# Kernel optimization log

Hardware: AMD Instinct MI355X
Metric: run time of the kernel (lower is better)

Reference implementation:

```python
import jax, jax.numpy as jnp
import numpy as np

K = 3          # kernel size
DIL = 1        # dilation
PAD = (K + (K - 1) * (DIL - 1)) // 2   # = 1
CENTER = (K * K - 1) // 2              # = 4
D_MIN = 0.0
D_MAX = 10.0
MIN_NGHBR = 4


def _unfold(x):
    """x: (B,C,H,W) -> patches (B,H,W,k*k,C), matching torch.nn.Unfold ordering."""
    b, c, h, w = x.shape
    xp = jnp.pad(x, ((0, 0), (0, 0), (PAD, PAD), (PAD, PAD)))
    # fixed k*k=9 taps: loop over the kernel window only (not data dims)
    pats = [xp[:, :, i * DIL:i * DIL + h, j * DIL:j * DIL + w]
            for i in range(K) for j in range(K)]
    p = jnp.stack(pats, axis=2)          # (B,C,kk,H,W)
    return p.transpose(0, 3, 4, 2, 1)    # (B,H,W,kk,C)


def setup_inputs() -> dict:
    key = jax.random.key(0)
    kxy, kz = jax.random.split(key)
    B, H, W = 4, 480, 640
    xy = jax.random.normal(kxy, (B, 2, H, W), dtype=jnp.float32)
    z = jax.random.uniform(kz, (B, 1, H, W), dtype=jnp.float32, minval=0.1, maxval=9.9)
    points = jnp.concatenate([xy, z], axis=1)  # (B,3,H,W)
    return {"points": points}


def reference(points):
    b, _, h, w = points.shape
    # 3x3 neighborhoods of 3D points: (B,H,W,9,3)
    A3 = _unfold(points)
    # depth-validity mask, unfolded over the same window: (B,H,W,9,1)
    depth = points[:, 2:3]
    valid = ((depth > D_MIN) & (depth < D_MAX)).astype(points.dtype)
    vc = _unfold(valid)
    # homogeneous design matrix A = [x y z 1], zeroed where neighbor invalid
    A = jnp.concatenate([A3, jnp.ones_like(A3[..., :1])], axis=-1)  # (B,H,W,9,4)
    A = jnp.where(vc > 0.5, A, jnp.zeros_like(A))
    # normal equations: per-pixel symmetric PSD 4x4
    AtA = jnp.einsum('bhwki,bhwkj->bhwij', A, A)
    # A^T A is symmetric PSD -> real eigensystem; eigh gives ascending eigvals,
    # so the null-space direction (smallest eigval) is column 0.
    eig_val, eig_vec = jnp.linalg.eigh(AtA)
    normal4 = eig_vec[..., :, 0]                      # (B,H,W,4)
    normal = normal4[..., :3].transpose(0, 3, 1, 2)   # (B,3,H,W)
    # F.normalize(p=2, dim=1, eps=1e-12)
    nrm = jnp.linalg.norm(normal, axis=1, keepdims=True)
    normal = normal / jnp.maximum(nrm, 1e-12)
    # orient toward the camera ray
    flip = jnp.sign(jnp.sum(normal * points, axis=1, keepdims=True))
    normal = normal * flip
    # validity masks
    vm1 = vc[:, :, :, CENTER, 0][:, None] > 0.5                 # center pixel valid
    vm2 = jnp.sum(vc[..., 0], axis=3)[:, None] >= MIN_NGHBR    # enough neighbors
    # vm3 (real eigensystem) is always True for the symmetric solve
    vm4 = jnp.linalg.norm(normal, axis=1, keepdims=True) > 0.5
    valid_mask = vm1 & vm2 & vm4
    return normal, valid_mask
```

## Files before the change

kernel.cpp:

```cpp
#include <hip/hip_runtime.h>

#define BB 4
#define HH 480
#define WW 640

__device__ __forceinline__ double det3d(double a, double b, double c,
                                        double d, double e, double f,
                                        double g, double h, double i) {
    return a * (e * i - f * h) - b * (d * i - f * g) + c * (d * h - e * g);
}

__device__ __forceinline__ double sdet3d(double a, double b, double c,
                                         double e, double f, double i) {
    return a * (e * i - f * f) + b * (2.0 * c * f - b * i) - c * c * e;
}

__device__ __forceinline__ double crcp(double d) {
    return (double)__builtin_amdgcn_rcpf((float)d);
}

__global__ __launch_bounds__(256) void d2n_kernel(const float* __restrict__ pts,
                                                  float* __restrict__ out) {
    int idx = blockIdx.x * 256 + threadIdx.x;
    if (idx >= BB * HH * WW) return;
    int x = idx % WW;
    int t1 = idx / WW;
    int y = t1 % HH;
    int b = t1 / HH;

    const size_t HW = (size_t)HH * WW;
    const float* xs = pts + ((size_t)b * 3 + 0) * HW;
    const float* ys = pts + ((size_t)b * 3 + 1) * HW;
    const float* zs = pts + ((size_t)b * 3 + 2) * HW;

    int row[3], col[3];
    bool rin[3], cin[3];
#pragma unroll
    for (int k = 0; k < 3; ++k) {
        int yy = y + k - 1, xx = x + k - 1;
        rin[k] = (unsigned)yy < HH;
        cin[k] = (unsigned)xx < WW;
        row[k] = min(max(yy, 0), HH - 1) * WW;
        col[k] = min(max(xx, 0), WW - 1);
    }
    float px[9], py[9], pz[9];
    bool inb[9];
#pragma unroll
    for (int i = 0; i < 9; ++i) {
        int r = i / 3, c = i % 3;
        int o = row[r] + col[c];
        inb[i] = rin[r] & cin[c];
        pz[i] = zs[o];
        px[i] = xs[o];
        py[i] = ys[o];
    }

    float sxx = 0.f, sxy = 0.f, sxz = 0.f, sx = 0.f;
    float syy = 0.f, syz = 0.f, sy = 0.f;
    float szz = 0.f, sz = 0.f, cnt = 0.f;
#pragma unroll
    for (int i = 0; i < 9; ++i) {
        float w = (inb[i] && pz[i] > 0.0f && pz[i] < 10.0f) ? 1.0f : 0.0f;
        float qx = px[i] * w, qy = py[i] * w, qz = pz[i] * w;
        sxx += qx * px[i]; sxy += qx * py[i]; sxz += qx * pz[i]; sx += qx;
        syy += qy * py[i]; syz += qy * pz[i]; sy += qy;
        szz += qz * pz[i]; sz += qz;
        cnt += w;
    }

    double tr = (double)sxx + (double)syy + (double)szz + (double)cnt;
    double it = crcp(tr);
    double m00 = sxx * it, m01 = sxy * it, m02 = sxz * it, m03 = sx * it;
    double m11 = syy * it, m12 = syz * it, m13 = sy * it;
    double m22 = szz * it, m23 = sz * it, m33 = cnt * it;

    double e1 = m00 + m11 + m22 + m33;
    double e2 = (m00 * m11 - m01 * m01) + (m00 * m22 - m02 * m02) +
                (m00 * m33 - m03 * m03) + (m11 * m22 - m12 * m12) +
                (m11 * m33 - m13 * m13) + (m22 * m33 - m23 * m23);
    double P0 = sdet3d(m11, m12, m13, m22, m23, m33);
    double P1 = sdet3d(m00, m02, m03, m22, m23, m33);
    double P2 = sdet3d(m00, m01, m03, m11, m13, m33);
    double P3 = sdet3d(m00, m01, m02, m11, m12, m22);
    double e3 = P0 + P1 + P2 + P3;
    double e4 = m00 * P0
              - m01 * det3d(m01, m12, m13, m02, m22, m23, m03, m23, m33)
              + m02 * det3d(m01, m11, m13, m02, m12, m23, m03, m13, m33)
              - m03 * det3d(m01, m11, m12, m02, m12, m22, m03, m13, m23);

    float e1f = (float)e1, e2f = (float)e2, e3f = (float)e3, e4f = (float)e4;
    float t31f = 3.0f * e1f, t22f = 2.0f * e2f;
    float lf = 0.0f;
#pragma unroll
    for (int itn = 0; itn < 8; ++itn) {
        float p  = (((lf - e1f) * lf + e2f) * lf - e3f) * lf + e4f;
        float dp = ((4.0f * lf - t31f) * lf + t22f) * lf - e3f;
        dp = fminf(dp, -1e-30f);
        lf = lf - p * __builtin_amdgcn_rcpf(dp);
        lf = fminf(fmaxf(lf, 0.0f), 0.26f);
    }
    double t31 = 3.0 * e1, t22 = 2.0 * e2;
    double lam = (double)lf;
#pragma unroll
    for (int itn = 0; itn < 5; ++itn) {
        double p  = (((lam - e1) * lam + e2) * lam - e3) * lam + e4;
        double dp = ((4.0 * lam - t31) * lam + t22) * lam - e3;
        dp = fmin(dp, -1e-30);
        lam = lam - p * crcp(dp);
        lam = fmin(fmax(lam, 0.0), 0.26);
    }

    double d0 = m00 - lam, d1 = m11 - lam, d2 = m22 - lam, d3 = m33 - lam;
    double C00 =  sdet3d(d1, m12, m13, d2, m23, d3);
    double C11 =  sdet3d(d0, m02, m03, d2, m23, d3);
    double C22 =  sdet3d(d0, m01, m03, d1, m13, d3);
    double C33 =  sdet3d(d0, m01, m02, d1, m12, d2);
    double C01 = -det3d(m01, m12, m13, m02, d2, m23, m03, m23, d3);
    double C02 =  det3d(m01, d1, m13, m02, m12, m23, m03, m13, d3);
    double C03 = -det3d(m01, d1, m12, m02, m12, d2, m03, m13, m23);
    double C12 = -det3d(d0, m01, m03, m02, m12, m23, m03, m13, d3);
    double C13 =  det3d(d0, m01, m02, m02, m12, d2, m03, m13, m23);
    double C23 = -det3d(d0, m01, m02, m01, d1, m12, m03, m13, m23);

    double best = fabs(C00);
    double vx = C00, vy = C01, vz = C02, vd = C00;
    double a1 = fabs(C11);
    if (a1 > best) { best = a1; vx = C01; vy = C11; vz = C12; vd = C11; }
    double a2 = fabs(C22);
    if (a2 > best) { best = a2; vx = C02; vy = C12; vz = C22; vd = C22; }
    double a3 = fabs(C33);
    if (a3 > best) { best = a3; vx = C03; vy = C13; vz = C23; vd = C33; }

    double sc = crcp(vd);
    float fx = (float)(vx * sc), fy = (float)(vy * sc), fz = (float)(vz * sc);

    float nd = fx * fx + fy * fy + fz * fz;
    float inv = __builtin_amdgcn_rsqf(fmaxf(nd, 1e-30f));
    float nx = fx * inv, ny = fy * inv, nz = fz * inv;

    int o = y * WW + x;
    float cx = px[4], cy = py[4], cz = pz[4];
    float dot = nx * cx + ny * cy + nz * cz;
    float sgn = (dot > 0.0f) ? 1.0f : ((dot < 0.0f) ? -1.0f : 0.0f);
    nx *= sgn; ny *= sgn; nz *= sgn;

    out[((size_t)b * 3 + 0) * HW + o] = nx;
    out[((size_t)b * 3 + 1) * HW + o] = ny;
    out[((size_t)b * 3 + 2) * HW + o] = nz;

    bool cvalid = (cz > 0.0f && cz < 10.0f);
    bool m = cvalid && (cnt >= 4.0f) && (nx * nx + ny * ny + nz * nz > 0.25f);
    out[(size_t)BB * 3 * HW + (size_t)b * HW + o] = m ? 1.0f : 0.0f;
}

extern "C" void kernel_launch(void* const* d_in, const int* in_sizes, int n_in,
                              void* d_out, int out_size, void* d_ws, size_t ws_size,
                              hipStream_t stream) {
    const float* pts = (const float*)d_in[0];
    float* out = (float*)d_out;
    int total = BB * HH * WW;
    d2n_kernel<<<(total + 255) / 256, 256, 0, stream>>>(pts, out);
}
```

Before: 85.51 us.

## Run eigen solve in fp32 with wave-uniform fp64 fallback for ill-conditioned pixels

Computes the characteristic polynomial, the Newton iterations and the adjugate eigenvector in single precision. A pixel is flagged when the derivative is near zero, lambda hits the clamp, or the vector norm is tiny. If any lane in the wavefront is flagged, the whole wavefront reruns the original double-precision path, and only flagged lanes take its result. This is meant to remove costly fp64 arithmetic from the common case, at the risk of accuracy loss where the float path passes the check but is imprecise, and of divergence cost when flagged pixels are spread across many wavefronts.

```diff
diff --git a/kernel.cpp b/kernel.cpp
--- a/kernel.cpp
+++ b/kernel.cpp
@@ -9,14 +9,21 @@
                                         double g, double h, double i) {
     return a * (e * i - f * h) - b * (d * i - f * g) + c * (d * h - e * g);
 }
-
 __device__ __forceinline__ double sdet3d(double a, double b, double c,
                                          double e, double f, double i) {
     return a * (e * i - f * f) + b * (2.0 * c * f - b * i) - c * c * e;
 }
-
 __device__ __forceinline__ double crcp(double d) {
     return (double)__builtin_amdgcn_rcpf((float)d);
+}
+__device__ __forceinline__ float det3f(float a, float b, float c,
+                                       float d, float e, float f,
+                                       float g, float h, float i) {
+    return a * (e * i - f * h) - b * (d * i - f * g) + c * (d * h - e * g);
+}
+__device__ __forceinline__ float sdet3f(float a, float b, float c,
+                                        float e, float f, float i) {
+    return a * (e * i - f * f) + b * (2.0f * c * f - b * i) - c * c * e;
 }
 
 __global__ __launch_bounds__(256) void d2n_kernel(const float* __restrict__ pts,
@@ -68,74 +75,126 @@
         cnt += w;
     }
 
-    double tr = (double)sxx + (double)syy + (double)szz + (double)cnt;
-    double it = crcp(tr);
-    double m00 = sxx * it, m01 = sxy * it, m02 = sxz * it, m03 = sx * it;
-    double m11 = syy * it, m12 = syz * it, m13 = sy * it;
-    double m22 = szz * it, m23 = sz * it, m33 = cnt * it;
-
-    double e1 = m00 + m11 + m22 + m33;
-    double e2 = (m00 * m11 - m01 * m01) + (m00 * m22 - m02 * m02) +
-                (m00 * m33 - m03 * m03) + (m11 * m22 - m12 * m12) +
-                (m11 * m33 - m13 * m13) + (m22 * m33 - m23 * m23);
-    double P0 = sdet3d(m11, m12, m13, m22, m23, m33);
-    double P1 = sdet3d(m00, m02, m03, m22, m23, m33);
-    double P2 = sdet3d(m00, m01, m03, m11, m13, m33);
-    double P3 = sdet3d(m00, m01, m02, m11, m12, m22);
-    double e3 = P0 + P1 + P2 + P3;
-    double e4 = m00 * P0
-              - m01 * det3d(m01, m12, m13, m02, m22, m23, m03, m23, m33)
-              + m02 * det3d(m01, m11, m13, m02, m12, m23, m03, m13, m33)
-              - m03 * det3d(m01, m11, m12, m02, m12, m22, m03, m13, m23);
-
-    float e1f = (float)e1, e2f = (float)e2, e3f = (float)e3, e4f = (float)e4;
+    float trf = sxx + syy + szz + cnt;
+    float itf = __builtin_amdgcn_rcpf(trf);
+    float f00 = sxx * itf, f01 = sxy * itf, f02 = sxz * itf, f03 = sx * itf;
+    float f11 = syy * itf, f12 = syz * itf, f13 = sy * itf;
+    float f22 = szz * itf, f23 = sz * itf, f33 = cnt * itf;
+
+    float e1f = f00 + f11 + f22 + f33;
+    float e2f = (f00 * f11 - f01 * f01) + (f00 * f22 - f02 * f02) +
+                (f00 * f33 - f03 * f03) + (f11 * f22 - f12 * f12) +
+                (f11 * f33 - f13 * f13) + (f22 * f33 - f23 * f23);
+    float Q0 = sdet3f(f11, f12, f13, f22, f23, f33);
+    float Q1 = sdet3f(f00, f02, f03, f22, f23, f33);
+    float Q2 = sdet3f(f00, f01, f03, f11, f13, f33);
+    float Q3 = sdet3f(f00, f01, f02, f11, f12, f22);
+    float e3f = Q0 + Q1 + Q2 + Q3;
+    float e4f = f00 * Q0
+              - f01 * det3f(f01, f12, f13, f02, f22, f23, f03, f23, f33)
+              + f02 * det3f(f01, f11, f13, f02, f12, f23, f03, f13, f33)
+              - f03 * det3f(f01, f11, f12, f02, f12, f22, f03, f13, f23);
+
     float t31f = 3.0f * e1f, t22f = 2.0f * e2f;
     float lf = 0.0f;
 #pragma unroll
-    for (int itn = 0; itn < 8; ++itn) {
+    for (int itn = 0; itn < 10; ++itn) {
         float p  = (((lf - e1f) * lf + e2f) * lf - e3f) * lf + e4f;
         float dp = ((4.0f * lf - t31f) * lf + t22f) * lf - e3f;
         dp = fminf(dp, -1e-30f);
         lf = lf - p * __builtin_amdgcn_rcpf(dp);
         lf = fminf(fmaxf(lf, 0.0f), 0.26f);
     }
-    double t31 = 3.0 * e1, t22 = 2.0 * e2;
-    double lam = (double)lf;
-#pragma unroll
-    for (int itn = 0; itn < 5; ++itn) {
-        double p  = (((lam - e1) * lam + e2) * lam - e3) * lam + e4;
-        double dp = ((4.0 * lam - t31) * lam + t22) * lam - e3;
-        dp = fmin(dp, -1e-30);
-        lam = lam - p * crcp(dp);
-        lam = fmin(fmax(lam, 0.0), 0.26);
-    }
-
-    double d0 = m00 - lam, d1 = m11 - lam, d2 = m22 - lam, d3 = m33 - lam;
-    double C00 =  sdet3d(d1, m12, m13, d2, m23, d3);
-    double C11 =  sdet3d(d0, m02, m03, d2, m23, d3);
-    double C22 =  sdet3d(d0, m01, m03, d1, m13, d3);
-    double C33 =  sdet3d(d0, m01, m02, d1, m12, d2);
-    double C01 = -det3d(m01, m12, m13, m02, d2, m23, m03, m23, d3);
-    double C02 =  det3d(m01, d1, m13, m02, m12, m23, m03, m13, d3);
-    double C03 = -det3d(m01, d1, m12, m02, m12, d2, m03, m13, m23);
-    double C12 = -det3d(d0, m01, m03, m02, m12, m23, m03, m13, d3);
-    double C13 =  det3d(d0, m01, m02, m02, m12, d2, m03, m13, m23);
-    double C23 = -det3d(d0, m01, m02, m01, d1, m12, m03, m13, m23);
-
-    double best = fabs(C00);
-    double vx = C00, vy = C01, vz = C02, vd = C00;
-    double a1 = fabs(C11);
-    if (a1 > best) { best = a1; vx = C01; vy = C11; vz = C12; vd = C11; }
-    double a2 = fabs(C22);
-    if (a2 > best) { best = a2; vx = C02; vy = C12; vz = C22; vd = C22; }
-    double a3 = fabs(C33);
-    if (a3 > best) { best = a3; vx = C03; vy = C13; vz = C23; vd = C33; }
-
-    double sc = crcp(vd);
-    float fx = (float)(vx * sc), fy = (float)(vy * sc), fz = (float)(vz * sc);
-
-    float nd = fx * fx + fy * fy + fz * fz;
-    float inv = __builtin_amdgcn_rsqf(fmaxf(nd, 1e-30f));
+    float dpf = ((4.0f * lf - t31f) * lf + t22f) * lf - e3f;
+
+    float g0 = f00 - lf, g1 = f11 - lf, g2 = f22 - lf, g3 = f33 - lf;
+    float B00 =  sdet3f(g1, f12, f13, g2, f23, g3);
+    float B11 =  sdet3f(g0, f02, f03, g2, f23, g3);
+    float B22 =  sdet3f(g0, f01, f03, g1, f13, g3);
+    float B33 =  sdet3f(g0, f01, f02, g1, f12, g2);
+    float B01 = -det3f(f01, f12, f13, f02, g2, f23, f03, f23, g3);
+    float B02 =  det3f(f01, g1, f13, f02, f12, f23, f03, f13, g3);
+    float B03 = -det3f(f01, g1, f12, f02, f12, g2, f03, f13, f23);
+    float B12 = -det3f(g0, f01, f03, f02, f12, f23, f03, f13, g3);
+    float B13 =  det3f(g0, f01, f02, f02, f12, g2, f03, f13, f23);
+    float B23 = -det3f(g0, f01, f02, f01, g1, f12, f03, f13, f23);
+
+    float bestf = fabsf(B00);
+    float fx = B00, fy = B01, fz = B02;
+    float b1a = fabsf(B11);
+    if (b1a > bestf) { bestf = b1a; fx = B01; fy = B11; fz = B12; }
+    float b2a = fabsf(B22);
+    if (b2a > bestf) { bestf = b2a; fx = B02; fy = B12; fz = B22; }
+    float b3a = fabsf(B33);
+    if (b3a > bestf) { bestf = b3a; fx = B03; fy = B13; fz = B23; }
+
+    float ndf = fx * fx + fy * fy + fz * fz;
+
+    bool flag = !(dpf < -2e-4f) || (lf > 0.2599f) || !(ndf > 1e-12f);
+
+    if (__any(flag)) {
+        double tr = (double)sxx + (double)syy + (double)szz + (double)cnt;
+        double it = crcp(tr);
+        double m00 = sxx * it, m01 = sxy * it, m02 = sxz * it, m03 = sx * it;
+        double m11 = syy * it, m12 = syz * it, m13 = sy * it;
+        double m22 = szz * it, m23 = sz * it, m33 = cnt * it;
+
+        double e1 = m00 + m11 + m22 + m33;
+        double e2 = (m00 * m11 - m01 * m01) + (m00 * m22 - m02 * m02) +
+                    (m00 * m33 - m03 * m03) + (m11 * m22 - m12 * m12) +
+                    (m11 * m33 - m13 * m13) + (m22 * m33 - m23 * m23);
+        double P0 = sdet3d(m11, m12, m13, m22, m23, m33);
+        double P1 = sdet3d(m00, m02, m03, m22, m23, m33);
+        double P2 = sdet3d(m00, m01, m03, m11, m13, m33);
+        double P3 = sdet3d(m00, m01, m02, m11, m12, m22);
+        double e3 = P0 + P1 + P2 + P3;
+        double e4 = m00 * P0
+                  - m01 * det3d(m01, m12, m13, m02, m22, m23, m03, m23, m33)
+                  + m02 * det3d(m01, m11, m13, m02, m12, m23, m03, m13, m33)
+                  - m03 * det3d(m01, m11, m12, m02, m12, m22, m03, m13, m23);
+
+        double t31 = 3.0 * e1, t22 = 2.0 * e2;
+        double lam = 0.0;
+#pragma unroll
+        for (int itn = 0; itn < 14; ++itn) {
+            double p  = (((lam - e1) * lam + e2) * lam - e3) * lam + e4;
+            double dp = ((4.0 * lam - t31) * lam + t22) * lam - e3;
+            dp = fmin(dp, -1e-30);
+            lam = lam - p * crcp(dp);
+            lam = fmin(fmax(lam, 0.0), 0.26);
+        }
+
+        double d0 = m00 - lam, d1 = m11 - lam, d2 = m22 - lam, d3 = m33 - lam;
+        double C00 =  sdet3d(d1, m12, m13, d2, m23, d3);
+        double C11 =  sdet3d(d0, m02, m03, d2, m23, d3);
+        double C22 =  sdet3d(d0, m01, m03, d1, m13, d3);
+        double C33 =  sdet3d(d0, m01, m02, d1, m12, d2);
+        double C01 = -det3d(m01, m12, m13, m02, d2, m23, m03, m23, d3);
+        double C02 =  det3d(m01, d1, m13, m02, m12, m23, m03, m13, d3);
+        double C03 = -det3d(m01, d1, m12, m02, m12, d2, m03, m13, m23);
+        double C12 = -det3d(d0, m01, m03, m02, m12, m23, m03, m13, d3);
+        double C13 =  det3d(d0, m01, m02, m02, m12, d2, m03, m13, m23);
+        double C23 = -det3d(d0, m01, m02, m01, d1, m12, m03, m13, m23);
+
+        double best = fabs(C00);
+        double vx = C00, vy = C01, vz = C02, vd = C00;
+        double a1 = fabs(C11);
+        if (a1 > best) { best = a1; vx = C01; vy = C11; vz = C12; vd = C11; }
+        double a2 = fabs(C22);
+        if (a2 > best) { best = a2; vx = C02; vy = C12; vz = C22; vd = C22; }
+        double a3 = fabs(C33);
+        if (a3 > best) { best = a3; vx = C03; vy = C13; vz = C23; vd = C33; }
+
+        double sc = crcp(vd);
+        float gx = (float)(vx * sc), gy = (float)(vy * sc), gz = (float)(vz * sc);
+
+        fx = flag ? gx : fx;
+        fy = flag ? gy : fy;
+        fz = flag ? gz : fz;
+        ndf = fx * fx + fy * fy + fz * fz;
+    }
+
+    float inv = __builtin_amdgcn_rsqf(fmaxf(ndf, 1e-30f));
     float nx = fx * inv, ny = fy * inv, nz = fz * inv;
 
     int o = y * WW + x;
```

Result: slower. 96.87 us (+13.3%).
